# Kernel optimization log

Hardware: AMD Instinct MI355X
Metric: run time of the kernel (lower is better)

Reference implementation:

```python
import jax, jax.numpy as jnp
import numpy as np
from jax import lax

FACTOR = 2
FIR = (1.0, 3.0, 3.0, 1.0)


def _fir_kernel():
    k1 = jnp.array(FIR, dtype=jnp.float32)
    k = jnp.outer(k1, k1)
    k = k / jnp.sum(k)
    return k * (FACTOR ** 2)  # gain=1, factor=2 -> x4


def _upfirdn2d(x, kernel, up, down, pad):
    # x: [N, C, H, W]; kernel: [kh, kw]; faithful to upfirdn2d_native:
    # upsample by zero-insertion (lhs_dilation), pad, convolve with flipped
    # kernel (F.conv2d is correlation of flipped kernel == true convolution),
    # then downsample by striding. lax.conv_general_dilated is correlation,
    # so pass the flipped kernel.
    C = x.shape[1]
    kflip = kernel[::-1, ::-1]
    w = jnp.tile(kflip[None, None], (C, 1, 1, 1))  # depthwise [C,1,kh,kw]
    return lax.conv_general_dilated(
        x, w,
        window_strides=(down, down),
        padding=[(pad[0], pad[1]), (pad[0], pad[1])],
        lhs_dilation=(up, up),
        feature_group_count=C,
        dimension_numbers=("NCHW", "OIHW", "NCHW"),
    )


def setup_inputs() -> dict:
    key = jax.random.key(0)
    k1, k2, k3 = jax.random.split(key, 3)
    N, C, H, W = 8, 256, 64, 64
    outC = 256
    hidden_states = jax.random.normal(k1, (N, C, H, W), dtype=jnp.float32)
    weight = jax.random.normal(k2, (outC, C, 3, 3), dtype=jnp.float32) * 0.05
    bias = jax.random.normal(k3, (outC,), dtype=jnp.float32)
    return {"hidden_states": hidden_states, "weight": weight, "bias": bias}


def reference(hidden_states, weight, bias):
    # FirUpsample2D.forward with use_conv=True, fir_kernel=(1,3,3,1), factor=2.
    k = _fir_kernel()  # [4, 4]
    convH, convW = weight.shape[2], weight.shape[3]
    pad_value = k.shape[0] - FACTOR - (convW - 1)  # = 0 here

    # The torch code flips+channel-swaps the weight then calls conv_transpose2d
    # (which itself flips and channel-swaps); the two cancel, so the net op is
    # plain cross-correlation of the ORIGINAL weight over the factor-dilated
    # input with (kH-1) padding on each side (output_padding == 0).
    x = lax.conv_general_dilated(
        hidden_states, weight,
        window_strides=(1, 1),
        padding=[(convH - 1, convH - 1), (convW - 1, convW - 1)],
        lhs_dilation=(FACTOR, FACTOR),
        dimension_numbers=("NCHW", "OIHW", "NCHW"),
    )  # [N, outC, (H-1)*2+3, (W-1)*2+3]

    out = _upfirdn2d(
        x, k, up=1, down=1,
        pad=((pad_value + 1) // 2 + FACTOR - 1, pad_value // 2 + 1),
    )  # [N, outC, 2H, 2W]

    return out + bias[None, :, None, None]
```

## Files before the change

kernel.cpp:

```cpp
#include <hip/hip_runtime.h>
#include <cstdint>
#include <cstddef>

typedef _Float16 f16;
typedef _Float16 f16x8 __attribute__((ext_vector_type(8)));
typedef float f32x4 __attribute__((ext_vector_type(4)));

#define AS1 __attribute__((address_space(1)))
#define AS3 __attribute__((address_space(3)))

__device__ __forceinline__ void gl_lds16(const void* g, void* l) {
  __builtin_amdgcn_global_load_lds((AS1 void*)g, (AS3 void*)l, 16u, 0, 0u);
}

__constant__ float c_tab[2][3][3] = {
  {{0.75f, 0.25f, 0.00f}, {0.25f, 0.75f, 0.75f}, {0.00f, 0.00f, 0.25f}},
  {{0.25f, 0.00f, 0.00f}, {0.75f, 0.75f, 0.25f}, {0.00f, 0.25f, 0.75f}}
};

__global__ __launch_bounds__(256) void prep_k(const float* __restrict__ W,
                                              const float* __restrict__ In,
                                              f16* __restrict__ Et,
                                              f16* __restrict__ Ah) {
  const int b = blockIdx.x;
  const int tid = threadIdx.x;
  if (b < 256) {
    const int oc = b;
    const int ic = tid;
    const int c = ic >> 5, icl = ic & 31;
    float w[9];
    const float* wp = W + ((size_t)oc * 256 + ic) * 9;
#pragma unroll
    for (int t = 0; t < 9; ++t) w[t] = wp[t];
#pragma unroll
    for (int py = 0; py < 2; ++py)
#pragma unroll
      for (int px = 0; px < 2; ++px) {
        const int jj = oc * 4 + py * 2 + px;
#pragma unroll
        for (int ay = 0; ay < 3; ++ay)
#pragma unroll
          for (int ax = 0; ax < 3; ++ax) {
            float s = 0.f;
#pragma unroll
            for (int iy = 0; iy < 3; ++iy)
#pragma unroll
              for (int ix = 0; ix < 3; ++ix)
                s += w[iy * 3 + ix] * c_tab[py][ay][iy] * c_tab[px][ax][ix];
            Et[((size_t)(((c * 3 + ay) * 3 + ax) * 1024 + jj)) * 32 + icl] = (f16)s;
          }
      }
  } else {
    const int bid2 = b - 256;
    const int icc = bid2 & 7;
    const int v = bid2 >> 3;
    const int n = v / 66;
    const int yp = v - n * 66;
    const int ic0 = icc * 32;
    const int icl = tid & 31, x8 = tid >> 5;
    f16* rowbase = Ah + ((size_t)(n * 66 + yp) * 66) * 256 + ic0;
    if (yp == 0 || yp == 65) {
#pragma unroll
      for (int i = 0; i < 9; ++i) {
        const int xp = i * 8 + x8;
        if (xp < 66) rowbase[(size_t)xp * 256 + icl] = (f16)0.f;
      }
    } else {
      const int y = yp - 1;
      __shared__ float tile[32][65];
      const int xl = tid & 63, icl4 = tid >> 6;
      const float* src = In + (((size_t)(n * 256 + ic0)) * 64 + y) * 64;
#pragma unroll
      for (int i = 0; i < 8; ++i) {
        const int icl_ = i * 4 + icl4;
        tile[icl_][xl] = src[(size_t)icl_ * 4096 + xl];
      }
      __syncthreads();
      f16* dst = rowbase + 256;
#pragma unroll
      for (int i = 0; i < 8; ++i) {
        const int x = i * 8 + x8;
        dst[(size_t)x * 256 + icl] = (f16)tile[icl][x];
      }
      if (x8 == 0) {
        rowbase[icl] = (f16)0.f;
        rowbase[(size_t)65 * 256 + icl] = (f16)0.f;
      }
    }
  }
}

__global__ __launch_bounds__(256) void gemm_k(const f16* __restrict__ Ah,
                                              const f16* __restrict__ Et,
                                              const float* __restrict__ bias,
                                              float* __restrict__ out) {
  __shared__ __align__(16) f16 lA[4224];
  __shared__ __align__(16) f16 lB[12288];
  const int tid = threadIdx.x;
  const int wave = tid >> 6;
  const int lane = tid & 63;
  const int bid = blockIdx.x;
  const int nt = bid & 7;
  const int mt = bid >> 3;
  const int m0 = mt * 128;
  const int jj0 = nt * 128;
  const int n = m0 >> 12;
  const int y0 = (m0 >> 6) & 63;

  int goA[2];
#pragma unroll
  for (int i = 0; i < 2; ++i) {
    const int s = wave * 2 + i;
    const int u = s * 16 + (lane >> 2);
    const int row = (u >= 66) ? 1 : 0;
    const int x = u - 66 * row;
    goA[i] = ((row * 66 + x) * 256 + (lane & 3) * 8) * 2;
  }
  const int goAt = ((66 + 62 + (lane >> 2)) * 256 + (lane & 3) * 8) * 2;
  int goB[6];
#pragma unroll
  for (int j = 0; j < 6; ++j) {
    const int t = wave + 4 * j;
    const int ax = t >> 3, sub = t & 7;
    goB[j] = (ax * 32768 + (sub * 16 + (lane >> 2)) * 32 + (lane & 3) * 8) * 2;
  }
  char* const lAb = (char*)lA;
  char* const lBb = (char*)lB;
  char* const dA0 = lAb + (wave * 2 + 0) * 1024;
  char* const dA1 = lAb + (wave * 2 + 1) * 1024;
  char* const dAt = lAb + 8192;

  const int wm = wave >> 1, wn = wave & 1;
  const int lr = lane & 15;
  const int base_a = wm * 4224 + lr * 64 + (lane >> 4) * 16;
  const int base_b = (wn * 64 + lr) * 64 + (lane >> 4) * 16;

  const char* const aN = (const char*)Ah + (size_t)(n * 66 + y0) * 33792;
  const char* const bE = (const char*)Et + (size_t)jj0 * 64;

  const f32x4 vzero = {0.f, 0.f, 0.f, 0.f};
  f32x4 acc[4][4];
#pragma unroll
  for (int i = 0; i < 4; ++i)
#pragma unroll
    for (int j = 0; j < 4; ++j) acc[i][j] = vzero;

#pragma unroll 1
  for (int c = 0; c < 8; ++c) {
#pragma unroll 1
    for (int ay = 0; ay < 3; ++ay) {
      const char* aP = aN + ay * 33792 + c * 64;
      const char* bP = bE + (size_t)(c * 3 + ay) * 196608;

      __syncthreads();
      gl_lds16(aP + goA[0], dA0);
      gl_lds16(aP + goA[1], dA1);
      if (wave == 3 && lane < 16) gl_lds16(aP + goAt, dAt);
#pragma unroll
      for (int j = 0; j < 6; ++j) gl_lds16(bP + goB[j], lBb + (wave + 4 * j) * 1024);
      __syncthreads();

#pragma unroll
      for (int ax = 0; ax < 3; ++ax) {
        f16x8 af[4], bf[4];
#pragma unroll
        for (int mi = 0; mi < 4; ++mi)
          af[mi] = *(const f16x8*)(lAb + base_a + (mi * 16 + ax) * 64);
#pragma unroll
        for (int ni = 0; ni < 4; ++ni)
          bf[ni] = *(const f16x8*)(lBb + base_b + ax * 8192 + ni * 1024);
#pragma unroll
        for (int mi = 0; mi < 4; ++mi)
#pragma unroll
          for (int ni = 0; ni < 4; ++ni)
            acc[mi][ni] =
                __builtin_amdgcn_mfma_f32_16x16x32_f16(af[mi], bf[ni], acc[mi][ni], 0, 0, 0);
      }
    }
  }

  const int yw = y0 + wm;
#pragma unroll
  for (int ni = 0; ni < 4; ++ni) {
    const int jj = jj0 + wn * 64 + ni * 16 + lr;
    const int oc = jj >> 2;
    const int py = (jj >> 1) & 1, px = jj & 1;
    const float bv = bias[oc];
    const int oy = 2 * yw + py;
    float* orow = out + ((size_t)(n * 256 + oc) * 128 + oy) * 128;
#pragma unroll
    for (int mi = 0; mi < 4; ++mi) {
      const int xb = mi * 16 + ((lane >> 4) << 2);
#pragma unroll
      for (int v = 0; v < 4; ++v) {
        orow[2 * (xb + v) + px] = acc[mi][ni][v] + bv;
      }
    }
  }
}

__global__ __launch_bounds__(256) void fallback_k(const float* __restrict__ In,
                                                  const float* __restrict__ W,
                                                  const float* __restrict__ bias,
                                                  float* __restrict__ out) {
  const size_t idx = (size_t)blockIdx.x * 256 + threadIdx.x;
  const int ox = (int)(idx & 127), oy = (int)((idx >> 7) & 127);
  const int oc = (int)((idx >> 14) & 255);
  const int n = (int)(idx >> 22);
  const int px = ox & 1, py = oy & 1;
  const int x = ox >> 1, y = oy >> 1;
  float cy[3][3], cx[3][3];
#pragma unroll
  for (int a = 0; a < 3; ++a)
#pragma unroll
    for (int i = 0; i < 3; ++i) {
      cy[a][i] = c_tab[py][a][i];
      cx[a][i] = c_tab[px][a][i];
    }
  float acc = 0.f;
  const float* wbase = W + (size_t)oc * 2304;
  for (int ic = 0; ic < 256; ++ic) {
    const float* ib = In + (((size_t)(n * 256 + ic)) * 64 + y) * 64 + x;
    float pin[3][3];
#pragma unroll
    for (int ay = 0; ay < 3; ++ay) {
      const int yy = y + ay - 1;
#pragma unroll
      for (int ax = 0; ax < 3; ++ax) {
        const int xx = x + ax - 1;
        pin[ay][ax] = (yy >= 0 && yy < 64 && xx >= 0 && xx < 64)
                          ? ib[(ay - 1) * 64 + (ax - 1)] : 0.f;
      }
    }
    const float* w = wbase + ic * 9;
    float U[3][3];
#pragma unroll
    for (int ay = 0; ay < 3; ++ay)
#pragma unroll
      for (int ix = 0; ix < 3; ++ix)
        U[ay][ix] = cx[0][ix] * pin[ay][0] + cx[1][ix] * pin[ay][1] + cx[2][ix] * pin[ay][2];
#pragma unroll
    for (int iy = 0; iy < 3; ++iy)
#pragma unroll
      for (int ix = 0; ix < 3; ++ix) {
        const float V = cy[0][iy] * U[0][ix] + cy[1][iy] * U[1][ix] + cy[2][iy] * U[2][ix];
        acc += w[iy * 3 + ix] * V;
      }
  }
  out[idx] = acc + bias[oc];
}

extern "C" void kernel_launch(void* const* d_in, const int* in_sizes, int n_in,
                              void* d_out, int out_size, void* d_ws, size_t ws_size,
                              hipStream_t stream) {
  const float* In = (const float*)d_in[0];
  const float* W = (const float*)d_in[1];
  const float* bias = (const float*)d_in[2];
  float* out = (float*)d_out;

  const size_t E_BYTES = (size_t)1024 * 2304 * 2;
  const size_t A_BYTES = (size_t)8 * 66 * 66 * 256 * 2;

  if (ws_size >= E_BYTES + A_BYTES) {
    f16* Et = (f16*)d_ws;
    f16* Ah = (f16*)((char*)d_ws + E_BYTES);
    prep_k<<<256 + 4224, 256, 0, stream>>>(W, In, Et, Ah);
    gemm_k<<<2048, 256, 0, stream>>>(Ah, Et, bias, out);
  } else {
    fallback_k<<<131072, 256, 0, stream>>>(In, W, bias, out);
  }
}
```

Before: 336.3 us.

## Read A operand directly from global and stage all 9 taps of B per channel chunk

The A (input) tile is no longer staged through LDS. Each wave now reads its A fragments straight from global memory, relying on cache reuse across the overlapping taps. The B (weight) tile for all nine ay/ax taps of a channel chunk is loaded into a larger 72KB LDS buffer at once, which cuts the barriers per chunk from six to two. The block index mapping is also swapped so consecutive blocks share the same weight tile, and launch bounds request 2 blocks per CU. The trade-offs are uncoalesced direct global loads for A, which the MFMA has to wait on, and higher LDS use per block.

```diff
diff --git a/kernel.cpp b/kernel.cpp
--- a/kernel.cpp
+++ b/kernel.cpp
@@ -90,53 +90,43 @@
   }
 }
 
-__global__ __launch_bounds__(256) void gemm_k(const f16* __restrict__ Ah,
-                                              const f16* __restrict__ Et,
-                                              const float* __restrict__ bias,
-                                              float* __restrict__ out) {
-  __shared__ __align__(16) f16 lA[4224];
-  __shared__ __align__(16) f16 lB[12288];
+__global__ __launch_bounds__(256, 2) void gemm_k(const f16* __restrict__ Ah,
+                                                 const f16* __restrict__ Et,
+                                                 const float* __restrict__ bias,
+                                                 float* __restrict__ out) {
+  __shared__ __align__(16) f16 lB[36864];
+  char* const lBb = (char*)lB;
   const int tid = threadIdx.x;
   const int wave = tid >> 6;
   const int lane = tid & 63;
   const int bid = blockIdx.x;
-  const int nt = bid & 7;
-  const int mt = bid >> 3;
+  const int mt = bid & 255;
+  const int nt = bid >> 8;
   const int m0 = mt * 128;
   const int jj0 = nt * 128;
   const int n = m0 >> 12;
   const int y0 = (m0 >> 6) & 63;
 
-  int goA[2];
-#pragma unroll
-  for (int i = 0; i < 2; ++i) {
-    const int s = wave * 2 + i;
-    const int u = s * 16 + (lane >> 2);
-    const int row = (u >= 66) ? 1 : 0;
-    const int x = u - 66 * row;
-    goA[i] = ((row * 66 + x) * 256 + (lane & 3) * 8) * 2;
-  }
-  const int goAt = ((66 + 62 + (lane >> 2)) * 256 + (lane & 3) * 8) * 2;
-  int goB[6];
-#pragma unroll
-  for (int j = 0; j < 6; ++j) {
-    const int t = wave + 4 * j;
-    const int ax = t >> 3, sub = t & 7;
-    goB[j] = (ax * 32768 + (sub * 16 + (lane >> 2)) * 32 + (lane & 3) * 8) * 2;
-  }
-  char* const lAb = (char*)lA;
-  char* const lBb = (char*)lB;
-  char* const dA0 = lAb + (wave * 2 + 0) * 1024;
-  char* const dA1 = lAb + (wave * 2 + 1) * 1024;
-  char* const dAt = lAb + 8192;
+  int goB[18];
+#pragma unroll
+  for (int j = 0; j < 18; ++j) {
+    const int s = wave + 4 * j;
+    const int ayax = s >> 3, sub = s & 7;
+    goB[j] = ayax * 65536 + (sub * 16 + (lane >> 2)) * 64 + (lane & 3) * 16;
+  }
 
   const int wm = wave >> 1, wn = wave & 1;
   const int lr = lane & 15;
-  const int base_a = wm * 4224 + lr * 64 + (lane >> 4) * 16;
-  const int base_b = (wn * 64 + lr) * 64 + (lane >> 4) * 16;
-
-  const char* const aN = (const char*)Ah + (size_t)(n * 66 + y0) * 33792;
+  const int il = lane >> 4;
+  int vOffA[4];
+#pragma unroll
+  for (int mi = 0; mi < 4; ++mi) {
+    const int ml = mi * 16 + lr;
+    vOffA[mi] = (wm * 66 + ml) * 512 + il * 16;
+  }
+  const char* const sA = (const char*)Ah + ((size_t)(n * 66 + y0) * 66) * 512;
   const char* const bE = (const char*)Et + (size_t)jj0 * 64;
+  const int rdB = lr * 64 + il * 16;
 
   const f32x4 vzero = {0.f, 0.f, 0.f, 0.f};
   f32x4 acc[4][4];
@@ -147,28 +137,26 @@
 
 #pragma unroll 1
   for (int c = 0; c < 8; ++c) {
-#pragma unroll 1
+    const char* bP = bE + (size_t)c * 589824;
+    __syncthreads();
+#pragma unroll
+    for (int j = 0; j < 18; ++j) gl_lds16(bP + goB[j], lBb + (wave + 4 * j) * 1024);
+    __syncthreads();
+
+    const char* aC = sA + c * 64;
+#pragma unroll
     for (int ay = 0; ay < 3; ++ay) {
-      const char* aP = aN + ay * 33792 + c * 64;
-      const char* bP = bE + (size_t)(c * 3 + ay) * 196608;
-
-      __syncthreads();
-      gl_lds16(aP + goA[0], dA0);
-      gl_lds16(aP + goA[1], dA1);
-      if (wave == 3 && lane < 16) gl_lds16(aP + goAt, dAt);
-#pragma unroll
-      for (int j = 0; j < 6; ++j) gl_lds16(bP + goB[j], lBb + (wave + 4 * j) * 1024);
-      __syncthreads();
-
 #pragma unroll
       for (int ax = 0; ax < 3; ++ax) {
+        const int ayax = ay * 3 + ax;
+        const char* aT = aC + (ay * 66 + ax) * 512;
         f16x8 af[4], bf[4];
 #pragma unroll
         for (int mi = 0; mi < 4; ++mi)
-          af[mi] = *(const f16x8*)(lAb + base_a + (mi * 16 + ax) * 64);
+          af[mi] = *(const f16x8*)(aT + vOffA[mi]);
 #pragma unroll
         for (int ni = 0; ni < 4; ++ni)
-          bf[ni] = *(const f16x8*)(lBb + base_b + ax * 8192 + ni * 1024);
+          bf[ni] = *(const f16x8*)(lBb + rdB + ayax * 8192 + wn * 4096 + ni * 1024);
 #pragma unroll
         for (int mi = 0; mi < 4; ++mi)
 #pragma unroll
@@ -190,7 +178,7 @@
     float* orow = out + ((size_t)(n * 256 + oc) * 128 + oy) * 128;
 #pragma unroll
     for (int mi = 0; mi < 4; ++mi) {
-      const int xb = mi * 16 + ((lane >> 4) << 2);
+      const int xb = mi * 16 + il * 4;
 #pragma unroll
       for (int v = 0; v < 4; ++v) {
         orow[2 * (xb + v) + px] = acc[mi][ni][v] + bv;
```

Measured after the change: 490.9 us. 1.46x slower.
